# Performance work log

Hardware: AMD Instinct MI355X
Metric: run time of the kernel (lower is better)

Reference implementation:

```python
import jax, jax.numpy as jnp
import numpy as np

DEPTH, IN_DIM, GRID, HID, BATCH = 3, 256, 64, 128, 4096
BN_EPS = 1e-5

def _lin(key, fi, fo):
    kw, kb = jax.random.split(key)
    bound = 1.0 / np.sqrt(fi)
    w = jax.random.uniform(kw, (fi, fo), jnp.float32, -bound, bound)
    b = jax.random.uniform(kb, (fo,), jnp.float32, -bound, bound)
    return w, b

def setup_inputs() -> dict:
    key = jax.random.key(0)
    ks = jax.random.split(key, 8)
    x = jax.random.normal(ks[0], (BATCH, IN_DIM), jnp.float32)
    fs = jax.random.normal(ks[1], (DEPTH, IN_DIM, GRID, HID), jnp.float32)
    grids = jnp.tile(jnp.linspace(0.0, 1.0, GRID, dtype=jnp.float32)[None, :], (DEPTH, 1))
    w1, b1 = _lin(ks[2], HID, HID * 2)
    w2, b2 = _lin(ks[3], HID * 2, HID)
    w3, b3 = _lin(ks[4], HID, HID // 2)
    w4, b4 = _lin(ks[5], HID // 2, 1)
    return {
        "x": x, "fs": fs, "grids": grids,
        "w1": w1, "b1": b1, "g1": jnp.ones(HID * 2), "be1": jnp.zeros(HID * 2),
        "w2": w2, "b2": b2, "g2": jnp.ones(HID), "be2": jnp.zeros(HID),
        "w3": w3, "b3": b3, "g3": jnp.ones(HID // 2), "be3": jnp.zeros(HID // 2),
        "w4": w4, "b4": b4,
    }

def _bn(a, g, b):
    # BatchNorm1d, training mode: biased batch variance, eps=1e-5
    m = a.mean(0)
    v = a.var(0)
    return (a - m) / jnp.sqrt(v + BN_EPS) * g + b

def reference(x, fs, grids, w1, b1, g1, be1, w2, b2, g2, be2, w3, b3, g3, be3, w4, b4):
    # per-feature min-max normalization over the batch
    zmin = x.min(0)
    zmax = x.max(0)
    z = (x - zmin) / (zmax - zmin + 1e-6)  # (B, I)
    h = jnp.zeros((x.shape[0], fs.shape[-1]), x.dtype)
    for i in range(fs.shape[0]):  # small fixed depth
        Bm = jax.nn.relu(z[:, :, None] - grids[i][None, None, :])  # (B, I, G)
        # fused multiply-reduce over grid AND input dims: (b,i,g) x (i,g,h) -> (b,h)
        h = h + jnp.einsum('big,igh->bh', Bm, fs[i])
    a = _bn(jax.nn.relu(h @ w1 + b1), g1, be1)
    a = _bn(jax.nn.relu(a @ w2 + b2), g2, be2)
    a = _bn(jax.nn.relu(a @ w3 + b3), g3, be3)
    return a @ w4 + b4  # (B, 1)
```

## Files before the change

### kernel.cpp

```cpp
#include <hip/hip_runtime.h>
#include <hip/hip_fp16.h>

#define BATCH 4096
#define IN_DIM 256
#define GRID_N 64
#define HID 128
#define GEMM_GB 128
constexpr float BN_EPS = 1e-5f;

typedef _Float16 h2 __attribute__((ext_vector_type(2)));
__device__ __forceinline__ h2 as_h2(unsigned u){ union {unsigned x; h2 h;} c; c.x = u; return c.h; }

static const size_t O_MMP  = 0;
static const size_t O_P1   = 32768;
static const size_t O_P2   = O_P1 + 262144;
static const size_t O_P3   = O_P2 + 131072;
static const size_t O_SS1  = O_P3 + 65536;
static const size_t O_SS2  = O_SS1 + 2048;
static const size_t O_SS3  = O_SS2 + 1024;
static const size_t O_STB  = O_SS3 + 1024;
static const size_t O_H    = O_STB + (size_t)256*65*128*4;
static const size_t O_A1   = O_H  + (size_t)4096*128*4;
static const size_t O_A2   = O_A1 + (size_t)4096*256*4;
static const size_t O_A3   = O_A2 + (size_t)4096*128*4;

__global__ __launch_bounds__(256) void k_prep(const float* __restrict__ x, const float* __restrict__ fs,
                                              const float* __restrict__ grids,
                                              float* __restrict__ mmp, unsigned* __restrict__ STb){
    const int tid = threadIdx.x;
    const int bid = blockIdx.x;
    if (bid < 16){
        const float* xp = x + (size_t)bid*256*IN_DIM + tid;
        float mn = 1e30f, mx = -1e30f;
        #pragma unroll 8
        for (int r = 0; r < 256; ++r){
            float v = xp[(size_t)r*IN_DIM];
            mn = fminf(mn, v); mx = fmaxf(mx, v);
        }
        mmp[(size_t)bid*512 + tid]       = mn;
        mmp[(size_t)bid*512 + 256 + tid] = mx;
        return;
    }
    const int i = (bid - 16)*2 + (tid >> 7);
    const int h = tid & 127;
    const float* f0 = fs + ((size_t)(0*IN_DIM + i)*GRID_N)*HID + h;
    const float* f1 = fs + ((size_t)(1*IN_DIM + i)*GRID_N)*HID + h;
    const float* f2 = fs + ((size_t)(2*IN_DIM + i)*GRID_N)*HID + h;
    unsigned* st = STb + (size_t)i*65*HID + h;
    float acc1 = 0.f, acc2 = 0.f;
    st[0] = 0u;
    #pragma unroll 4
    for (int k = 0; k < 64; ++k){
        float fv = f0[(size_t)k*HID] + f1[(size_t)k*HID] + f2[(size_t)k*HID];
        float g  = grids[k];
        acc1 += fv;
        acc2  = fmaf(g, fv, acc2);
        __half2 hh = __halves2half2(__float2half_rn(acc1), __float2half_rn(-acc2));
        st[(size_t)(k+1)*HID] = *reinterpret_cast<unsigned*>(&hh);
    }
}

__global__ __launch_bounds__(128) void k_gather(const float* __restrict__ x, const float* __restrict__ mmp,
                                                const unsigned* __restrict__ STb, float* __restrict__ h){
    __shared__ float s_zmin[256], s_inv[256];
    __shared__ uint2 pre[2][256];
    const int tid = threadIdx.x;
    const int b0  = blockIdx.x * 2;

    for (int f = tid; f < 256; f += 128){
        float mn = 1e30f, mx = -1e30f;
        #pragma unroll
        for (int p = 0; p < 16; ++p){
            mn = fminf(mn, mmp[(size_t)p*512 + f]);
            mx = fmaxf(mx, mmp[(size_t)p*512 + 256 + f]);
        }
        s_zmin[f] = mn;
        s_inv[f]  = 1.0f / (mx - mn + 1e-6f);
    }
    __syncthreads();

    for (int idx = tid; idx < 2*256; idx += 128){
        int bl = idx >> 8, i = idx & 255;
        float z = (x[(size_t)(b0 + bl)*IN_DIM + i] - s_zmin[i]) * s_inv[i];
        int K0 = (int)(z * 63.0f) + 1;
        K0 = max(1, min(63, K0));
        unsigned off = ((unsigned)(i*65 + K0)) << 9;
        __half2 zh = __halves2half2(__float2half_rn(z), __float2half_rn(1.0f));
        pre[bl][i] = make_uint2(*reinterpret_cast<unsigned*>(&zh), off);
    }
    __syncthreads();

    const int w  = tid >> 6;
    const int l  = tid & 63;
    const int hl = l & 31;
    const int hi = l >> 5;
    const char* base = (const char*)STb + (size_t)hl * 16;
    const uint2* pp = &pre[w][hi * 128];
    float acc0 = 0.f, acc1 = 0.f, acc2 = 0.f, acc3 = 0.f;
    #pragma unroll 8
    for (int ii = 0; ii < 128; ++ii){
        uint2 p = pp[ii];
        uint4 u = *reinterpret_cast<const uint4*>(base + p.y);
        h2 zz = as_h2(p.x);
        acc0 = __builtin_amdgcn_fdot2(zz, as_h2(u.x), acc0, false);
        acc1 = __builtin_amdgcn_fdot2(zz, as_h2(u.y), acc1, false);
        acc2 = __builtin_amdgcn_fdot2(zz, as_h2(u.z), acc2, false);
        acc3 = __builtin_amdgcn_fdot2(zz, as_h2(u.w), acc3, false);
    }
    acc0 += __shfl(acc0, hl + 32);
    acc1 += __shfl(acc1, hl + 32);
    acc2 += __shfl(acc2, hl + 32);
    acc3 += __shfl(acc3, hl + 32);
    if (hi == 0){
        *reinterpret_cast<float4*>(&h[(size_t)(b0 + w)*HID + 4*hl]) =
            make_float4(acc0, acc1, acc2, acc3);
    }
}

__global__ __launch_bounds__(256) void k_stats(const float* __restrict__ part, float* __restrict__ stats,
                                               int twoN){
    int j = blockIdx.x*256 + threadIdx.x;
    if (j >= twoN) return;
    float s = 0.f;
    #pragma unroll 8
    for (int p = 0; p < GEMM_GB; ++p) s += part[(size_t)p*twoN + j];
    stats[j] = s;
}

template<int BN_IN>
__global__ __launch_bounds__(256) void k_gemm(const float* __restrict__ A, const float* __restrict__ W,
                                              const float* __restrict__ bias,
                                              const float* __restrict__ instats,
                                              const float* __restrict__ gam, const float* __restrict__ bet,
                                              float* __restrict__ C, float* __restrict__ outpart,
                                              int K, int N){
    __shared__ float As[32][33];
    __shared__ float Ws[32][64];
    __shared__ float bnsc[256], bnsh[256];
    __shared__ float red[16][16][8];

    const int tid = threadIdx.x;
    const int n0  = blockIdx.x * 64;
    const int b0  = blockIdx.y * 32;

    if (BN_IN){
        for (int k = tid; k < K; k += 256){
            float m  = instats[k]     * (1.0f/BATCH);
            float v  = instats[K + k] * (1.0f/BATCH) - m*m;
            float rs = rsqrtf(v + BN_EPS);
            float sc = gam[k]*rs;
            bnsc[k] = sc;
            bnsh[k] = fmaf(-m, sc, bet[k]);
        }
        __syncthreads();
    }

    const int nt = tid & 15;
    const int bt = tid >> 4;
    float acc[2][4];
    #pragma unroll
    for (int r = 0; r < 2; ++r)
        #pragma unroll
        for (int j = 0; j < 4; ++j) acc[r][j] = 0.f;

    for (int kc = 0; kc < K; kc += 32){
        #pragma unroll
        for (int idx = tid; idx < 32*32; idx += 256){
            int r = idx >> 5, k = idx & 31;
            float a = A[(size_t)(b0 + r)*K + kc + k];
            if (BN_IN) a = fmaf(a, bnsc[kc + k], bnsh[kc + k]);
            As[r][k] = a;
        }
        #pragma unroll
        for (int idx = tid; idx < 32*64; idx += 256){
            int k = idx >> 6, n = idx & 63;
            Ws[k][n] = W[(size_t)(kc + k)*N + n0 + n];
        }
        __syncthreads();
        #pragma unroll
        for (int k = 0; k < 32; ++k){
            float4 w = *reinterpret_cast<const float4*>(&Ws[k][nt*4]);
            float a0 = As[bt*2+0][k], a1 = As[bt*2+1][k];
            acc[0][0] = fmaf(a0, w.x, acc[0][0]); acc[0][1] = fmaf(a0, w.y, acc[0][1]);
            acc[0][2] = fmaf(a0, w.z, acc[0][2]); acc[0][3] = fmaf(a0, w.w, acc[0][3]);
            acc[1][0] = fmaf(a1, w.x, acc[1][0]); acc[1][1] = fmaf(a1, w.y, acc[1][1]);
            acc[1][2] = fmaf(a1, w.z, acc[1][2]); acc[1][3] = fmaf(a1, w.w, acc[1][3]);
        }
        __syncthreads();
    }

    float bs[4];
    #pragma unroll
    for (int j = 0; j < 4; ++j) bs[j] = bias[n0 + nt*4 + j];
    float lsum[4] = {0,0,0,0}, lsq[4] = {0,0,0,0};
    #pragma unroll
    for (int r = 0; r < 2; ++r){
        int brow = b0 + bt*2 + r;
        float vv[4];
        #pragma unroll
        for (int j = 0; j < 4; ++j){
            float v1 = acc[r][j] + bs[j];
            v1 = fmaxf(v1, 0.f);
            vv[j] = v1;
            lsum[j] += v1;
            lsq[j]  = fmaf(v1, v1, lsq[j]);
        }
        *reinterpret_cast<float4*>(&C[(size_t)brow*N + n0 + nt*4]) =
            make_float4(vv[0], vv[1], vv[2], vv[3]);
    }
    #pragma unroll
    for (int j = 0; j < 4; ++j){ red[bt][nt][j] = lsum[j]; red[bt][nt][4+j] = lsq[j]; }
    __syncthreads();
    for (int s = 8; s > 0; s >>= 1){
        if (bt < s){
            #pragma unroll
            for (int f = 0; f < 8; ++f) red[bt][nt][f] += red[bt+s][nt][f];
        }
        __syncthreads();
    }
    if (bt == 0){
        float* op = outpart + (size_t)blockIdx.y*(2*N);
        #pragma unroll
        for (int j = 0; j < 4; ++j){
            op[n0 + nt*4 + j]     = red[0][nt][j];
            op[N + n0 + nt*4 + j] = red[0][nt][4+j];
        }
    }
}

__global__ __launch_bounds__(256) void k_final(const float* __restrict__ A3, const float* __restrict__ ss3,
                                               const float* __restrict__ g3, const float* __restrict__ be3,
                                               const float* __restrict__ w4, const float* __restrict__ b4,
                                               float* __restrict__ out){
    __shared__ float sc[64], sh[64];
    int t = threadIdx.x;
    if (t < 64){
        float m  = ss3[t]      * (1.0f/BATCH);
        float v  = ss3[64 + t] * (1.0f/BATCH) - m*m;
        float rs = rsqrtf(v + BN_EPS);
        float g  = g3[t]*rs;
        sc[t] = g * w4[t];
        sh[t] = fmaf(-m, g, be3[t]) * w4[t];
    }
    __syncthreads();
    int row = blockIdx.x*256 + t;
    const float* a = A3 + (size_t)row*64;
    float acc = b4[0];
    #pragma unroll
    for (int k = 0; k < 64; ++k){
        acc = fmaf(a[k], sc[k], acc);
        acc += sh[k];
    }
    out[row] = acc;
}

extern "C" void kernel_launch(void* const* d_in, const int* in_sizes, int n_in,
                              void* d_out, int out_size, void* d_ws, size_t ws_size,
                              hipStream_t stream){
    const float* x     = (const float*)d_in[0];
    const float* fs    = (const float*)d_in[1];
    const float* grids = (const float*)d_in[2];
    const float* w1 = (const float*)d_in[3];  const float* b1 = (const float*)d_in[4];
    const float* g1 = (const float*)d_in[5];  const float* be1= (const float*)d_in[6];
    const float* w2 = (const float*)d_in[7];  const float* b2 = (const float*)d_in[8];
    const float* g2 = (const float*)d_in[9];  const float* be2= (const float*)d_in[10];
    const float* w3 = (const float*)d_in[11]; const float* b3 = (const float*)d_in[12];
    const float* g3 = (const float*)d_in[13]; const float* be3= (const float*)d_in[14];
    const float* w4 = (const float*)d_in[15]; const float* b4 = (const float*)d_in[16];
    float* out = (float*)d_out;

    char* ws = (char*)d_ws;
    float* mmp    = (float*)(ws + O_MMP);
    float* p1     = (float*)(ws + O_P1);
    float* p2     = (float*)(ws + O_P2);
    float* p3     = (float*)(ws + O_P3);
    float* ss1    = (float*)(ws + O_SS1);
    float* ss2    = (float*)(ws + O_SS2);
    float* ss3    = (float*)(ws + O_SS3);
    unsigned* STb = (unsigned*)(ws + O_STB);
    float* h      = (float*)(ws + O_H);
    float* A1     = (float*)(ws + O_A1);
    float* A2     = (float*)(ws + O_A2);
    float* A3     = (float*)(ws + O_A3);

    k_prep<<<144, 256, 0, stream>>>(x, fs, grids, mmp, STb);
    k_gather<<<2048, 128, 0, stream>>>(x, mmp, STb, h);
    k_gemm<0><<<dim3(4, 128), 256, 0, stream>>>(h,  w1, b1, nullptr, nullptr, nullptr, A1, p1, 128, 256);
    k_stats<<<2, 256, 0, stream>>>(p1, ss1, 512);
    k_gemm<1><<<dim3(2, 128), 256, 0, stream>>>(A1, w2, b2, ss1, g1, be1,            A2, p2, 256, 128);
    k_stats<<<1, 256, 0, stream>>>(p2, ss2, 256);
    k_gemm<1><<<dim3(1, 128), 256, 0, stream>>>(A2, w3, b3, ss2, g2, be2,            A3, p3, 128, 64);
    k_stats<<<1, 256, 0, stream>>>(p3, ss3, 128);
    k_final<<<16, 256, 0, stream>>>(A3, ss3, g3, be3, w4, b4, out);
}
```

Baseline: 119.4 us.

## Halve GEMM batch tile to double block count and fold last stats into final

The MLP GEMM kernels now process 16 rows per block instead of 32, with a K-chunk of 64, doubling the grid along the batch to raise occupancy on the many compute units. The partial-stats buffers double to match. The separate reduction launch for the third layer's BatchNorm stats is removed, and k_final reduces the 256 partials itself. The trade-off is more partial-stat traffic, each k_final block repeating that reduction, and less register reuse per thread.

Measured after the change: 119.6 us. About the same (+0.1%).

```diff
diff --git a/kernel.cpp b/kernel.cpp
--- a/kernel.cpp
+++ b/kernel.cpp
@@ -5,7 +5,7 @@
 #define IN_DIM 256
 #define GRID_N 64
 #define HID 128
-#define GEMM_GB 128
+#define GEMM_GB 256
 constexpr float BN_EPS = 1e-5f;
 
 typedef _Float16 h2 __attribute__((ext_vector_type(2)));
@@ -13,12 +13,11 @@
 
 static const size_t O_MMP  = 0;
 static const size_t O_P1   = 32768;
-static const size_t O_P2   = O_P1 + 262144;
-static const size_t O_P3   = O_P2 + 131072;
-static const size_t O_SS1  = O_P3 + 65536;
+static const size_t O_P2   = O_P1 + 524288;
+static const size_t O_P3   = O_P2 + 262144;
+static const size_t O_SS1  = O_P3 + 131072;
 static const size_t O_SS2  = O_SS1 + 2048;
-static const size_t O_SS3  = O_SS2 + 1024;
-static const size_t O_STB  = O_SS3 + 1024;
+static const size_t O_STB  = O_SS2 + 2048;
 static const size_t O_H    = O_STB + (size_t)256*65*128*4;
 static const size_t O_A1   = O_H  + (size_t)4096*128*4;
 static const size_t O_A2   = O_A1 + (size_t)4096*256*4;
@@ -134,14 +133,14 @@
                                               const float* __restrict__ gam, const float* __restrict__ bet,
                                               float* __restrict__ C, float* __restrict__ outpart,
                                               int K, int N){
-    __shared__ float As[32][33];
-    __shared__ float Ws[32][64];
+    __shared__ float As[16][64];
+    __shared__ float Ws[64][64];
     __shared__ float bnsc[256], bnsh[256];
     __shared__ float red[16][16][8];
 
     const int tid = threadIdx.x;
     const int n0  = blockIdx.x * 64;
-    const int b0  = blockIdx.y * 32;
+    const int b0  = blockIdx.y * 16;
 
     if (BN_IN){
         for (int k = tid; k < K; k += 256){
@@ -157,59 +156,45 @@
 
     const int nt = tid & 15;
     const int bt = tid >> 4;
-    float acc[2][4];
-    #pragma unroll
-    for (int r = 0; r < 2; ++r)
-        #pragma unroll
-        for (int j = 0; j < 4; ++j) acc[r][j] = 0.f;
-
-    for (int kc = 0; kc < K; kc += 32){
-        #pragma unroll
-        for (int idx = tid; idx < 32*32; idx += 256){
-            int r = idx >> 5, k = idx & 31;
+    float acc[4] = {0.f, 0.f, 0.f, 0.f};
+
+    for (int kc = 0; kc < K; kc += 64){
+        #pragma unroll
+        for (int idx = tid; idx < 16*64; idx += 256){
+            int r = idx >> 6, k = idx & 63;
             float a = A[(size_t)(b0 + r)*K + kc + k];
             if (BN_IN) a = fmaf(a, bnsc[kc + k], bnsh[kc + k]);
             As[r][k] = a;
         }
         #pragma unroll
-        for (int idx = tid; idx < 32*64; idx += 256){
+        for (int idx = tid; idx < 64*64; idx += 256){
             int k = idx >> 6, n = idx & 63;
             Ws[k][n] = W[(size_t)(kc + k)*N + n0 + n];
         }
         __syncthreads();
         #pragma unroll
-        for (int k = 0; k < 32; ++k){
+        for (int k = 0; k < 64; ++k){
             float4 w = *reinterpret_cast<const float4*>(&Ws[k][nt*4]);
-            float a0 = As[bt*2+0][k], a1 = As[bt*2+1][k];
-            acc[0][0] = fmaf(a0, w.x, acc[0][0]); acc[0][1] = fmaf(a0, w.y, acc[0][1]);
-            acc[0][2] = fmaf(a0, w.z, acc[0][2]); acc[0][3] = fmaf(a0, w.w, acc[0][3]);
-            acc[1][0] = fmaf(a1, w.x, acc[1][0]); acc[1][1] = fmaf(a1, w.y, acc[1][1]);
-            acc[1][2] = fmaf(a1, w.z, acc[1][2]); acc[1][3] = fmaf(a1, w.w, acc[1][3]);
-        }
-        __syncthreads();
-    }
-
-    float bs[4];
+            float a0 = As[bt][k];
+            acc[0] = fmaf(a0, w.x, acc[0]); acc[1] = fmaf(a0, w.y, acc[1]);
+            acc[2] = fmaf(a0, w.z, acc[2]); acc[3] = fmaf(a0, w.w, acc[3]);
+        }
+        __syncthreads();
+    }
+
+    float vv[4];
     #pragma unroll
-    for (int j = 0; j < 4; ++j) bs[j] = bias[n0 + nt*4 + j];
-    float lsum[4] = {0,0,0,0}, lsq[4] = {0,0,0,0};
+    for (int j = 0; j < 4; ++j){
+        float v1 = acc[j] + bias[n0 + nt*4 + j];
+        vv[j] = fmaxf(v1, 0.f);
+    }
+    *reinterpret_cast<float4*>(&C[(size_t)(b0 + bt)*N + n0 + nt*4]) =
+        make_float4(vv[0], vv[1], vv[2], vv[3]);
     #pragma unroll
-    for (int r = 0; r < 2; ++r){
-        int brow = b0 + bt*2 + r;
-        float vv[4];
-        #pragma unroll
-        for (int j = 0; j < 4; ++j){
-            float v1 = acc[r][j] + bs[j];
-            v1 = fmaxf(v1, 0.f);
-            vv[j] = v1;
-            lsum[j] += v1;
-            lsq[j]  = fmaf(v1, v1, lsq[j]);
-        }
-        *reinterpret_cast<float4*>(&C[(size_t)brow*N + n0 + nt*4]) =
-            make_float4(vv[0], vv[1], vv[2], vv[3]);
-    }
-    #pragma unroll
-    for (int j = 0; j < 4; ++j){ red[bt][nt][j] = lsum[j]; red[bt][nt][4+j] = lsq[j]; }
+    for (int j = 0; j < 4; ++j){
+        red[bt][nt][j]   = vv[j];
+        red[bt][nt][4+j] = vv[j]*vv[j];
+    }
     __syncthreads();
     for (int s = 8; s > 0; s >>= 1){
         if (bt < s){
@@ -228,15 +213,26 @@
     }
 }
 
-__global__ __launch_bounds__(256) void k_final(const float* __restrict__ A3, const float* __restrict__ ss3,
+__global__ __launch_bounds__(256) void k_final(const float* __restrict__ A3, const float* __restrict__ p3,
                                                const float* __restrict__ g3, const float* __restrict__ be3,
                                                const float* __restrict__ w4, const float* __restrict__ b4,
                                                float* __restrict__ out){
+    __shared__ float psum[2][128];
     __shared__ float sc[64], sh[64];
-    int t = threadIdx.x;
+    const int t = threadIdx.x;
+    {
+        int j = t & 127, half = t >> 7;
+        float s = 0.f;
+        #pragma unroll 8
+        for (int p = half*128; p < half*128 + 128; ++p) s += p3[(size_t)p*128 + j];
+        psum[half][j] = s;
+    }
+    __syncthreads();
     if (t < 64){
-        float m  = ss3[t]      * (1.0f/BATCH);
-        float v  = ss3[64 + t] * (1.0f/BATCH) - m*m;
+        float s  = psum[0][t]      + psum[1][t];
+        float ss = psum[0][64 + t] + psum[1][64 + t];
+        float m  = s  * (1.0f/BATCH);
+        float v  = ss * (1.0f/BATCH) - m*m;
         float rs = rsqrtf(v + BN_EPS);
         float g  = g3[t]*rs;
         sc[t] = g * w4[t];
@@ -276,7 +272,6 @@
     float* p3     = (float*)(ws + O_P3);
     float* ss1    = (float*)(ws + O_SS1);
     float* ss2    = (float*)(ws + O_SS2);
-    float* ss3    = (float*)(ws + O_SS3);
     unsigned* STb = (unsigned*)(ws + O_STB);
     float* h      = (float*)(ws + O_H);
     float* A1     = (float*)(ws + O_A1);
@@ -285,11 +280,10 @@
 
     k_prep<<<144, 256, 0, stream>>>(x, fs, grids, mmp, STb);
     k_gather<<<2048, 128, 0, stream>>>(x, mmp, STb, h);
-    k_gemm<0><<<dim3(4, 128), 256, 0, stream>>>(h,  w1, b1, nullptr, nullptr, nullptr, A1, p1, 128, 256);
+    k_gemm<0><<<dim3(4, 256), 256, 0, stream>>>(h,  w1, b1, nullptr, nullptr, nullptr, A1, p1, 128, 256);
     k_stats<<<2, 256, 0, stream>>>(p1, ss1, 512);
-    k_gemm<1><<<dim3(2, 128), 256, 0, stream>>>(A1, w2, b2, ss1, g1, be1,            A2, p2, 256, 128);
+    k_gemm<1><<<dim3(2, 256), 256, 0, stream>>>(A1, w2, b2, ss1, g1, be1,            A2, p2, 256, 128);
     k_stats<<<1, 256, 0, stream>>>(p2, ss2, 256);
-    k_gemm<1><<<dim3(1, 128), 256, 0, stream>>>(A2, w3, b3, ss2, g2, be2,            A3, p3, 128, 64);
-    k_stats<<<1, 256, 0, stream>>>(p3, ss3, 128);
-    k_final<<<16, 256, 0, stream>>>(A3, ss3, g3, be3, w4, b4, out);
-}
+    k_gemm<1><<<dim3(1, 256), 256, 0, stream>>>(A2, w3, b3, ss2, g2, be2,            A3, p3, 128, 64);
+    k_final<<<16, 256, 0, stream>>>(A3, p3, g3, be3, w4, b4, out);
+}
```
